# Performance work log

Measured on AMD Instinct MI355X. Metric: run time of the kernel, lower is better.

## Reference

```python
import jax, jax.numpy as jnp
import numpy as np

N, E, G = 50000, 800000, 64
IN, EDGE = 128, 16
HID, H = 32, 4
FHID, HF = 64, 4
OUT = 16
NEG_SLOPE = 0.2


def _segment_softmax(logits, seg, num):
    m = jax.ops.segment_max(logits, seg, num_segments=num)
    m = jnp.where(jnp.isfinite(m), m, 0.0)
    p = jnp.exp(logits - m[seg])
    s = jax.ops.segment_sum(p, seg, num_segments=num)
    return p / (s[seg] + 1e-16)


def gatv2(x, src, dst, eattr, Wl, bl, Wr, br, We, att, bias, concat):
    # PyG GATv2Conv with add_self_loops=True (edge_attr fill_value='mean')
    n = x.shape[0]
    heads, ch = att.shape
    ones = jnp.ones((src.shape[0],), x.dtype)
    cnt = jax.ops.segment_sum(ones, dst, num_segments=n)
    mean_attr = jax.ops.segment_sum(eattr, dst, num_segments=n) / jnp.maximum(cnt, 1.0)[:, None]
    loop = jnp.arange(n)
    s = jnp.concatenate([src, loop])
    d = jnp.concatenate([dst, loop])
    ea = jnp.concatenate([eattr, mean_attr], axis=0)
    xl = (x @ Wl + bl).reshape(n, heads, ch)   # lin_l (source)
    xr = (x @ Wr + br).reshape(n, heads, ch)   # lin_r (target)
    ee = (ea @ We).reshape(-1, heads, ch)      # lin_edge (no bias)
    z = jax.nn.leaky_relu(xl[s] + xr[d] + ee, NEG_SLOPE)  # [E+N, H, C]
    logits = jnp.einsum('ehc,hc->eh', z, att)
    alpha = _segment_softmax(logits, d, n)
    out = jax.ops.segment_sum(alpha[:, :, None] * xl[s], d, num_segments=n)  # [N, H, C]
    out = out.reshape(n, heads * ch) if concat else out.mean(axis=1)
    return out + bias


def _forward(x, edge_attr, src, dst, batch,
             Wl0, bl0, Wr0, br0, We0, att0, bo0,
             Wlh, blh, Wrh, brh, Weh, atth, boh,
             Wlf, blf, Wrf, brf, Wef, attf, bof,
             Wlin, blin):
    h1 = jax.nn.relu(gatv2(x, src, dst, edge_attr, Wl0, bl0, Wr0, br0, We0, att0, bo0, True))
    h2 = jax.nn.relu(gatv2(h1, src, dst, edge_attr, Wlh, blh, Wrh, brh, Weh, atth, boh, True))
    h3 = jax.nn.relu(gatv2(h2, src, dst, edge_attr, Wlf, blf, Wrf, brf, Wef, attf, bof, False))
    # global_mean_pool over graphs
    gsum = jax.ops.segment_sum(h3, batch, num_segments=G)
    gcnt = jax.ops.segment_sum(jnp.ones((h3.shape[0],), h3.dtype), batch, num_segments=G)
    g = gsum / jnp.maximum(gcnt, 1.0)[:, None]
    return g @ Wlin + blin  # final_dropout inactive in eval mode


def setup_inputs():
    key = jax.random.key(0)
    ks = jax.random.split(key, 20)
    def p(i, shape, fan_in):
        return jax.random.normal(ks[i], shape, jnp.float32) / np.sqrt(fan_in)
    z = lambda *s: jnp.zeros(s, jnp.float32)
    return {
        'x': jax.random.normal(ks[0], (N, IN), jnp.float32),
        'edge_index': jax.random.randint(ks[1], (2, E), 0, N),
        'batch': jnp.sort(jax.random.randint(ks[2], (N,), 0, G)),
        'edge_attr': jax.random.normal(ks[3], (E, EDGE), jnp.float32),
        'Wl0': p(4, (IN, H * HID), IN), 'bl0': z(H * HID),
        'Wr0': p(5, (IN, H * HID), IN), 'br0': z(H * HID),
        'We0': p(6, (EDGE, H * HID), EDGE), 'att0': p(7, (H, HID), HID), 'bo0': z(H * HID),
        'Wlh': p(8, (H * HID, H * HID), H * HID), 'blh': z(H * HID),
        'Wrh': p(9, (H * HID, H * HID), H * HID), 'brh': z(H * HID),
        'Weh': p(10, (EDGE, H * HID), EDGE), 'atth': p(11, (H, HID), HID), 'boh': z(H * HID),
        'Wlf': p(12, (H * HID, HF * FHID), H * HID), 'blf': z(HF * FHID),
        'Wrf': p(13, (H * HID, HF * FHID), H * HID), 'brf': z(HF * FHID),
        'Wef': p(14, (EDGE, HF * FHID), EDGE), 'attf': p(15, (HF, FHID), FHID), 'bof': z(FHID),
        'Wlin': p(16, (FHID, OUT), FHID), 'blin': z(OUT),
    }


def reference(x, edge_index, batch, edge_attr, Wl0, bl0, Wr0, br0, We0, att0, bo0, Wlh, blh, Wrh, brh, Weh, atth, boh, Wlf, blf, Wrf, brf, Wef, attf, bof, Wlin, blin):
    return _forward(x, edge_attr, edge_index[0], edge_index[1], batch,
                    Wl0, bl0, Wr0, br0, We0, att0, bo0,
                    Wlh, blh, Wrh, brh, Weh, atth, boh,
                    Wlf, blf, Wrf, brf, Wef, attf, bof,
                    Wlin, blin)
```

## Files before the change

### kernel.cpp

```cpp
#include <hip/hip_runtime.h>
#include <cstddef>

#define NSLOPE 0.2f

constexpr int NN = 50000;
constexpr int EE = 800000;
constexpr int GG = 64;
constexpr int SCAN_B = 1024;

typedef unsigned short ushort_t;
typedef unsigned int uint_t;
typedef __bf16 bhalf;
typedef bhalf bhalf8 __attribute__((ext_vector_type(8)));
typedef float floatx4 __attribute__((ext_vector_type(4)));
typedef _Float16 half_t;
typedef half_t half2_t __attribute__((ext_vector_type(2)));

__device__ __forceinline__ ushort_t f2b(float f) {
  unsigned int u = __float_as_uint(f);
  unsigned int r = (u + 0x7fffu + ((u >> 16) & 1u)) >> 16;
  return (ushort_t)r;
}
__device__ __forceinline__ float b2f(ushort_t b) {
  return __uint_as_float(((unsigned int)b) << 16);
}
__device__ __forceinline__ uint_t packh2(float a, float b) {
  half2_t h = {(half_t)a, (half_t)b};
  return __builtin_bit_cast(uint_t, h);
}
__device__ __forceinline__ float dot2acc(uint_t ea, half2_t w, float c) {
  half2_t a = __builtin_bit_cast(half2_t, ea);
#if __has_builtin(__builtin_amdgcn_fdot2)
  return __builtin_amdgcn_fdot2(a, w, c, false);
#else
  return c + (float)a.x * (float)w.x + (float)a.y * (float)w.y;
#endif
}

__device__ __forceinline__ float red16(float x) {
  int v = __builtin_bit_cast(int, x);
  x += __builtin_bit_cast(float, __builtin_amdgcn_update_dpp(0, v, 0xB1, 0xF, 0xF, true));
  v = __builtin_bit_cast(int, x);
  x += __builtin_bit_cast(float, __builtin_amdgcn_update_dpp(0, v, 0x4E, 0xF, 0xF, true));
  v = __builtin_bit_cast(int, x);
  x += __builtin_bit_cast(float, __builtin_amdgcn_update_dpp(0, v, 0x124, 0xF, 0xF, true));
  v = __builtin_bit_cast(int, x);
  x += __builtin_bit_cast(float, __builtin_amdgcn_update_dpp(0, v, 0x128, 0xF, 0xF, true));
  return x;
}

__global__ void hist_kernel(const int* __restrict__ dst, int* __restrict__ hist, int E) {
  int e = blockIdx.x * blockDim.x + threadIdx.x;
  if (e < E) atomicAdd(&hist[dst[e]], 1);
}

__global__ void scan_block_kernel(const int* __restrict__ in, int* __restrict__ out,
                                  int* __restrict__ bsum, int n) {
  __shared__ int tmp[SCAN_B];
  int gid = blockIdx.x * SCAN_B + threadIdx.x;
  int v = (gid < n) ? in[gid] : 0;
  tmp[threadIdx.x] = v;
  __syncthreads();
  for (int off = 1; off < SCAN_B; off <<= 1) {
    int t = (threadIdx.x >= off) ? tmp[threadIdx.x - off] : 0;
    __syncthreads();
    tmp[threadIdx.x] += t;
    __syncthreads();
  }
  if (gid < n) out[gid] = tmp[threadIdx.x];
  if (threadIdx.x == SCAN_B - 1) bsum[blockIdx.x] = tmp[threadIdx.x];
}

__global__ void scan_totals_kernel(const int* __restrict__ bsum, int* __restrict__ boff, int nb) {
  if (blockIdx.x == 0 && threadIdx.x == 0) {
    int run = 0;
    for (int i = 0; i < nb; ++i) { boff[i] = run; run += bsum[i]; }
  }
}

__global__ void add_offsets_kernel(int* __restrict__ rowptr, const int* __restrict__ boff,
                                   int* __restrict__ cursor, int n) {
  int gid = blockIdx.x * SCAN_B + threadIdx.x;
  if (gid == 0) { rowptr[0] = 0; cursor[0] = 0; }
  if (gid < n) {
    int v = rowptr[1 + gid] + boff[blockIdx.x];
    rowptr[1 + gid] = v;
    if (1 + gid < n) cursor[1 + gid] = v;
  }
}

__global__ void scatter_fused_kernel(const int* __restrict__ dst, const int* __restrict__ src,
                                     const float* __restrict__ eattr, int* __restrict__ cursor,
                                     int* __restrict__ srcp, uint_t* __restrict__ eah, int E) {
  int e = blockIdx.x * blockDim.x + threadIdx.x;
  if (e >= E) return;
  const float4* a = reinterpret_cast<const float4*>(eattr + (size_t)e * 16);
  float4 f0 = a[0], f1 = a[1], f2 = a[2], f3 = a[3];
  int pos = atomicAdd(&cursor[dst[e]], 1);
  srcp[pos] = src[e];
  uint4 o0 = make_uint4(packh2(f0.x, f0.y), packh2(f0.z, f0.w),
                        packh2(f1.x, f1.y), packh2(f1.z, f1.w));
  uint4 o1 = make_uint4(packh2(f2.x, f2.y), packh2(f2.z, f2.w),
                        packh2(f3.x, f3.y), packh2(f3.z, f3.w));
  uint4* b = reinterpret_cast<uint4*>(eah + (size_t)pos * 8);
  b[0] = o0; b[1] = o1;
}

__global__ __launch_bounds__(256) void mean_attr_kernel(
    const int* __restrict__ rowptr, const uint_t* __restrict__ eah,
    uint_t* __restrict__ meanattr_h, int N) {
  const int lane = threadIdx.x & 63;
  int d = blockIdx.x * (blockDim.x >> 6) + (threadIdx.x >> 6);
  if (d >= N) return;
  int beg = rowptr[d], end = rowptr[d + 1];
  int k2 = lane & 7;
  int sub = lane >> 3;
  float ax = 0.f, ay = 0.f;
  for (int j = beg + sub; j < end; j += 8) {
    half2_t h = __builtin_bit_cast(half2_t, eah[(size_t)j * 8 + k2]);
    ax += (float)h.x; ay += (float)h.y;
  }
  ax += __shfl_xor(ax, 8);  ay += __shfl_xor(ay, 8);
  ax += __shfl_xor(ax, 16); ay += __shfl_xor(ay, 16);
  ax += __shfl_xor(ax, 32); ay += __shfl_xor(ay, 32);
  if (sub == 0) {
    int c = end - beg; if (c < 1) c = 1;
    float inv = 1.f / (float)c;
    meanattr_h[(size_t)d * 8 + k2] = packh2(ax * inv, ay * inv);
  }
}

__global__ void f2b_kernel(const float* __restrict__ in, ushort_t* __restrict__ out, int n4) {
  int i = blockIdx.x * blockDim.x + threadIdx.x;
  if (i >= n4) return;
  float4 v = reinterpret_cast<const float4*>(in)[i];
  ushort4 o = make_ushort4(f2b(v.x), f2b(v.y), f2b(v.z), f2b(v.w));
  reinterpret_cast<ushort4*>(out)[i] = o;
}

__global__ void prep_w_kernel(const float* W0, ushort_t* T0, int n0,
                              const float* W1, ushort_t* T1, int n1,
                              const float* W2, ushort_t* T2, int n2,
                              const float* W3, ushort_t* T3, int n3,
                              const float* W4, ushort_t* T4, int n4,
                              const float* W5, ushort_t* T5, int n5) {
  const float* W; ushort_t* T; int Nc;
  switch (blockIdx.y) {
    case 0: W = W0; T = T0; Nc = n0; break;
    case 1: W = W1; T = T1; Nc = n1; break;
    case 2: W = W2; T = T2; Nc = n2; break;
    case 3: W = W3; T = T3; Nc = n3; break;
    case 4: W = W4; T = T4; Nc = n4; break;
    default: W = W5; T = T5; Nc = n5; break;
  }
  int idx = blockIdx.x * blockDim.x + threadIdx.x;
  if (idx >= Nc * 128) return;
  int n = idx >> 7, k = idx & 127;
  T[idx] = f2b(W[(size_t)k * Nc + n]);
}

__global__ void prep_we_kernel(const float* We0, const float* att0, uint_t* w0, float* a0,
                               const float* We1, const float* att1, uint_t* w1, float* a1,
                               const float* We2, const float* att2, uint_t* w2, float* a2) {
  const float* We; const float* att; uint_t* wp; float* ap; int C;
  switch (blockIdx.y) {
    case 0: We = We0; att = att0; wp = w0; ap = a0; C = 128; break;
    case 1: We = We1; att = att1; wp = w1; ap = a1; C = 128; break;
    default: We = We2; att = att2; wp = w2; ap = a2; C = 256; break;
  }
  int idx = blockIdx.x * blockDim.x + threadIdx.x;
  if (idx >= 9 * C) return;
  if (idx < 8 * C) {
    int sh = (C == 256) ? 8 : 7;
    int k2 = idx >> sh, ch = idx & (C - 1);
    wp[idx] = packh2(We[(size_t)(2 * k2) * C + ch], We[(size_t)(2 * k2 + 1) * C + ch]);
  } else {
    int ch = idx - 8 * C;
    ap[ch] = att[ch] * 1.44269504f;
  }
}

__global__ __launch_bounds__(256) void gemm_bt_dual_bf16(
    const ushort_t* __restrict__ Xb,
    const ushort_t* __restrict__ Wt0, const float* __restrict__ b0, ushort_t* __restrict__ Y0,
    const ushort_t* __restrict__ Wt1, const float* __restrict__ b1, ushort_t* __restrict__ Y1,
    int M, int Nc) {
  constexpr int K = 128, BM = 128, LDT = 136;
  __shared__ ushort_t Als[BM * LDT];
  __shared__ ushort_t Bls[BM * LDT];
  int nb = Nc >> 7;
  int half = blockIdx.y / nb;
  int cb = blockIdx.y % nb;
  const ushort_t* Wt = half ? Wt1 : Wt0;
  const float* bias = half ? b1 : b0;
  ushort_t* Y = half ? Y1 : Y0;
  int r0 = blockIdx.x * BM;
  int col0 = cb * 128;
  int tid = threadIdx.x;
  {
    int rl = tid >> 5;
    int kq = (tid & 31) * 4;
#pragma unroll
    for (int s = 0; s < 16; ++s) {
      int row = rl + s * 8;
      int grow = r0 + row;
      ushort4 v = make_ushort4(0, 0, 0, 0);
      if (grow < M) v = *reinterpret_cast<const ushort4*>(Xb + (size_t)grow * K + kq);
      *reinterpret_cast<ushort4*>(&Als[row * LDT + kq]) = v;
      ushort4 wv = *reinterpret_cast<const ushort4*>(Wt + (size_t)(col0 + row) * K + kq);
      *reinterpret_cast<ushort4*>(&Bls[row * LDT + kq]) = wv;
    }
  }
  __syncthreads();
  int lane = tid & 63;
  int w = tid >> 6;
  int m0 = (w >> 1) * 64;
  int n0 = (w & 1) * 64;
  int rin = lane & 15, quad = lane >> 4;
  floatx4 acc[4][4];
#pragma unroll
  for (int i = 0; i < 4; ++i)
#pragma unroll
    for (int j = 0; j < 4; ++j) acc[i][j] = (floatx4){0.f, 0.f, 0.f, 0.f};
#pragma unroll
  for (int kt = 0; kt < 4; ++kt) {
    int ko = kt * 32 + quad * 8;
    bhalf8 af[4], bf[4];
#pragma unroll
    for (int i = 0; i < 4; ++i)
      af[i] = *reinterpret_cast<const bhalf8*>(&Als[(m0 + i * 16 + rin) * LDT + ko]);
#pragma unroll
    for (int i = 0; i < 4; ++i)
      bf[i] = *reinterpret_cast<const bhalf8*>(&Bls[(n0 + i * 16 + rin) * LDT + ko]);
#pragma unroll
    for (int mi = 0; mi < 4; ++mi)
#pragma unroll
      for (int ni = 0; ni < 4; ++ni)
        acc[mi][ni] = __builtin_amdgcn_mfma_f32_16x16x32_bf16(af[mi], bf[ni], acc[mi][ni], 0, 0, 0);
  }
#pragma unroll
  for (int ni = 0; ni < 4; ++ni) {
    int gcol = col0 + n0 + ni * 16 + rin;
    float bb = bias[gcol];
#pragma unroll
    for (int mi = 0; mi < 4; ++mi) {
      int growb = r0 + m0 + mi * 16 + quad * 4;
#pragma unroll
      for (int r = 0; r < 4; ++r) {
        int grow = growb + r;
        if (grow < M) Y[(size_t)grow * Nc + gcol] = f2b(acc[mi][ni][r] + bb);
      }
    }
  }
}

template <int VPL>
__device__ __forceinline__ void loadb(const ushort_t* p, float* v) {
  if constexpr (VPL == 2) {
    ushort2 t = *reinterpret_cast<const ushort2*>(p);
    v[0] = b2f(t.x); v[1] = b2f(t.y);
  } else {
    ushort4 t = *reinterpret_cast<const ushort4*>(p);
    v[0] = b2f(t.x); v[1] = b2f(t.y); v[2] = b2f(t.z); v[3] = b2f(t.w);
  }
}
template <int VPL>
__device__ __forceinline__ void storeb(ushort_t* p, const float* v) {
  if constexpr (VPL == 2) {
    *reinterpret_cast<ushort2*>(p) = make_ushort2(f2b(v[0]), f2b(v[1]));
  } else {
    *reinterpret_cast<ushort4*>(p) = make_ushort4(f2b(v[0]), f2b(v[1]), f2b(v[2]), f2b(v[3]));
  }
}

template <int VPL>
__device__ __forceinline__ float lrelu_dot(const float* xv, const float* rv,
                                           const half2_t (*wepk)[VPL], const float* areg,
                                           const uint_t* ea) {
  float part = 0.f;
#pragma unroll
  for (int j = 0; j < VPL; ++j) {
    float z = xv[j] + rv[j];
#pragma unroll
    for (int k2 = 0; k2 < 8; ++k2) z = dot2acc(ea[k2], wepk[k2][j], z);
    float zl = fmaxf(z, NSLOPE * z);
    part = fmaf(zl, areg[j], part);
  }
  return red16(part);
}

template <int EB, int VPL, int C>
__device__ __forceinline__ void process_group(
    const int* __restrict__ srcp, const uint_t* __restrict__ eah, int j,
    const ushort_t* __restrict__ xl, int lane, const float* rv,
    const half2_t (*wepk)[VPL], const float* areg,
    float& s, float* acc) {
  int sn[EB];
#pragma unroll
  for (int u = 0; u < EB; ++u) sn[u] = srcp[j + u];
  float xv[EB][VPL];
#pragma unroll
  for (int u = 0; u < EB; ++u) loadb<VPL>(xl + (size_t)sn[u] * C + lane * VPL, xv[u]);
  float lg[EB];
#pragma unroll
  for (int u = 0; u < EB; ++u) {
    const uint4* ap4 = reinterpret_cast<const uint4*>(eah + (size_t)(j + u) * 8);
    uint4 e0 = ap4[0], e1 = ap4[1];
    uint_t ea[8] = {e0.x, e0.y, e0.z, e0.w, e1.x, e1.y, e1.z, e1.w};
    lg[u] = lrelu_dot<VPL>(xv[u], rv, wepk, areg, ea);
  }
  float p[EB], ps = 0.f;
#pragma unroll
  for (int u = 0; u < EB; ++u) { p[u] = exp2f(lg[u]); ps += p[u]; }
  s += ps;
#pragma unroll
  for (int jj = 0; jj < VPL; ++jj) {
    float t = p[0] * xv[0][jj];
#pragma unroll
    for (int u = 1; u < EB; ++u) t = fmaf(p[u], xv[u][jj], t);
    acc[jj] += t;
  }
}

template <int VPL, int C>
__device__ __forceinline__ void process_edge(
    int sn, const uint_t* ea,
    const ushort_t* __restrict__ xl, int lane, const float* rv,
    const half2_t (*wepk)[VPL], const float* areg,
    float& s, float* acc) {
  float xv[VPL];
  loadb<VPL>(xl + (size_t)sn * C + lane * VPL, xv);
  float lg = lrelu_dot<VPL>(xv, rv, wepk, areg, ea);
  float p = exp2f(lg);
  s += p;
#pragma unroll
  for (int jj = 0; jj < VPL; ++jj) acc[jj] = fmaf(p, xv[jj], acc[jj]);
}

template <int C, bool FINAL>
__global__ __launch_bounds__(256) void gat_fused_kernel(
    const int* __restrict__ rowptr,
    const int* __restrict__ srcp, const uint_t* __restrict__ eah,
    const uint_t* __restrict__ meanattr_h,
    const ushort_t* __restrict__ xl, const ushort_t* __restrict__ xr,
    const uint_t* __restrict__ wep,
    const float* __restrict__ atts,
    const float* __restrict__ bias, ushort_t* __restrict__ hout, int N) {
  constexpr int VPL = C / 64;
  const int lane = threadIdx.x & 63;
  int d = __builtin_amdgcn_readfirstlane(blockIdx.x * (blockDim.x >> 6) + (threadIdx.x >> 6));
  if (d >= N) return;

  half2_t wepk[8][VPL];
  float areg[VPL];
#pragma unroll
  for (int k2 = 0; k2 < 8; ++k2)
#pragma unroll
    for (int jj = 0; jj < VPL; ++jj)
      wepk[k2][jj] = __builtin_bit_cast(half2_t, wep[k2 * C + lane * VPL + jj]);
#pragma unroll
  for (int jj = 0; jj < VPL; ++jj) areg[jj] = atts[lane * VPL + jj];

  int beg = rowptr[d], end = rowptr[d + 1];
  float rv[VPL];
  loadb<VPL>(xr + (size_t)d * C + lane * VPL, rv);

  float s = 0.f;
  float acc[VPL];
#pragma unroll
  for (int jj = 0; jj < VPL; ++jj) acc[jj] = 0.f;

  int j = beg;
  if constexpr (C == 128) {
    for (; j + 8 <= end; j += 8)
      process_group<8, VPL, C>(srcp, eah, j, xl, lane, rv, wepk, areg, s, acc);
  }
  for (; j + 4 <= end; j += 4)
    process_group<4, VPL, C>(srcp, eah, j, xl, lane, rv, wepk, areg, s, acc);
  for (; j + 2 <= end; j += 2)
    process_group<2, VPL, C>(srcp, eah, j, xl, lane, rv, wepk, areg, s, acc);
  for (; j < end; ++j)
    process_group<1, VPL, C>(srcp, eah, j, xl, lane, rv, wepk, areg, s, acc);

  {
    const uint4* mp4 = reinterpret_cast<const uint4*>(meanattr_h + (size_t)d * 8);
    uint4 e0 = mp4[0], e1 = mp4[1];
    uint_t ea[8] = {e0.x, e0.y, e0.z, e0.w, e1.x, e1.y, e1.z, e1.w};
    process_edge<VPL, C>(d, ea, xl, lane, rv, wepk, areg, s, acc);
  }

  float inv = 1.f / (s + 1e-16f);
  if constexpr (!FINAL) {
    float res[VPL];
#pragma unroll
    for (int jj = 0; jj < VPL; ++jj) {
      float v = acc[jj] * inv + bias[lane * VPL + jj];
      res[jj] = v > 0.f ? v : 0.f;
    }
    storeb<VPL>(hout + (size_t)d * C + lane * VPL, res);
  } else {
    float v[VPL];
#pragma unroll
    for (int jj = 0; jj < VPL; ++jj) v[jj] = acc[jj] * inv;
#pragma unroll
    for (int jj = 0; jj < VPL; ++jj) {
      v[jj] += __shfl_xor(v[jj], 16);
      v[jj] += __shfl_xor(v[jj], 32);
    }
    if (lane < 16) {
      float res[VPL];
#pragma unroll
      for (int jj = 0; jj < VPL; ++jj) {
        float val = 0.25f * v[jj] + bias[lane * VPL + jj];
        res[jj] = val > 0.f ? val : 0.f;
      }
      storeb<VPL>(hout + (size_t)d * 64 + lane * VPL, res);
    }
  }
}

__global__ __launch_bounds__(256) void pool_kernel(
    const ushort_t* __restrict__ h3, const int* __restrict__ batch,
    float* __restrict__ gsum, float* __restrict__ gcnt, int N) {
  const int lane = threadIdx.x & 63;
  const int w = blockIdx.x * (blockDim.x >> 6) + (threadIdx.x >> 6);
  const int nw = gridDim.x * (blockDim.x >> 6);
  const int chunk = (N + nw - 1) / nw;
  int i0 = w * chunk;
  int i1 = i0 + chunk; if (i1 > N) i1 = N;
  if (i0 >= i1) return;
  int cur = batch[i0];
  float acc = 0.f;
  int cnt = 0;
  for (int i = i0; i < i1; ++i) {
    int g = batch[i];
    if (g != cur) {
      atomicAdd(&gsum[(size_t)cur * 64 + lane], acc);
      if (lane == 0) atomicAdd(&gcnt[cur], (float)cnt);
      acc = 0.f; cnt = 0; cur = g;
    }
    acc += b2f(h3[(size_t)i * 64 + lane]);
    ++cnt;
  }
  atomicAdd(&gsum[(size_t)cur * 64 + lane], acc);
  if (lane == 0) atomicAdd(&gcnt[cur], (float)cnt);
}

__global__ void final_kernel(const float* __restrict__ gsum, const float* __restrict__ gcnt,
                             const float* __restrict__ Wlin, const float* __restrict__ blin,
                             float* __restrict__ out) {
  int idx = blockIdx.x * blockDim.x + threadIdx.x;
  if (idx >= GG * 16) return;
  int g = idx >> 4, o = idx & 15;
  float c = gcnt[g];
  c = c > 1.f ? c : 1.f;
  float inv = 1.f / c;
  float acc = blin[o];
  for (int f = 0; f < 64; ++f) acc = fmaf(gsum[(size_t)g * 64 + f] * inv, Wlin[f * 16 + o], acc);
  out[idx] = acc;
}

extern "C" void kernel_launch(void* const* d_in, const int* in_sizes, int n_in,
                              void* d_out, int out_size, void* d_ws, size_t ws_size,
                              hipStream_t stream) {
  (void)in_sizes; (void)n_in; (void)out_size; (void)ws_size;
  const float* x     = (const float*)d_in[0];
  const int*   eidx  = (const int*)d_in[1];
  const int*   batch = (const int*)d_in[2];
  const float* eattr = (const float*)d_in[3];
  const float* Wl0 = (const float*)d_in[4];  const float* bl0 = (const float*)d_in[5];
  const float* Wr0 = (const float*)d_in[6];  const float* br0 = (const float*)d_in[7];
  const float* We0 = (const float*)d_in[8];  const float* att0 = (const float*)d_in[9];
  const float* bo0 = (const float*)d_in[10];
  const float* Wlh = (const float*)d_in[11]; const float* blh = (const float*)d_in[12];
  const float* Wrh = (const float*)d_in[13]; const float* brh = (const float*)d_in[14];
  const float* Weh = (const float*)d_in[15]; const float* atth = (const float*)d_in[16];
  const float* boh = (const float*)d_in[17];
  const float* Wlf = (const float*)d_in[18]; const float* blf = (const float*)d_in[19];
  const float* Wrf = (const float*)d_in[20]; const float* brf = (const float*)d_in[21];
  const float* Wef = (const float*)d_in[22]; const float* attf = (const float*)d_in[23];
  const float* bof = (const float*)d_in[24];
  const float* Wlin = (const float*)d_in[25]; const float* blin = (const float*)d_in[26];

  const int* src = eidx;
  const int* dst = eidx + EE;

  char* ws = (char*)d_ws;
  size_t off = 0;
  auto take = [&](size_t bytes) -> void* {
    void* p = ws + off;
    off += (bytes + 1023) & ~(size_t)1023;
    return p;
  };
  ushort_t* xl     = (ushort_t*)take((size_t)NN * 256 * 2);
  ushort_t* xr     = (ushort_t*)take((size_t)NN * 256 * 2);
  ushort_t* hb     = (ushort_t*)take((size_t)NN * 128 * 2);
  ushort_t* xb     = (ushort_t*)take((size_t)NN * 128 * 2);
  uint_t* meanattr_h = (uint_t*)take((size_t)NN * 8 * 4);
  int* hist        = (int*)take((size_t)NN * 4);
  int* rowptr      = (int*)take((size_t)(NN + 1) * 4);
  int* cursor      = (int*)take((size_t)NN * 4);
  int* bsum        = (int*)take(256);
  int* boff        = (int*)take(256);
  float* gsum      = (float*)take((size_t)GG * 64 * 4);
  float* gcnt      = (float*)take((size_t)GG * 4);
  ushort_t* wtl0   = (ushort_t*)take((size_t)128 * 128 * 2);
  ushort_t* wtr0   = (ushort_t*)take((size_t)128 * 128 * 2);
  ushort_t* wtlh   = (ushort_t*)take((size_t)128 * 128 * 2);
  ushort_t* wtrh   = (ushort_t*)take((size_t)128 * 128 * 2);
  ushort_t* wtlf   = (ushort_t*)take((size_t)256 * 128 * 2);
  ushort_t* wtrf   = (ushort_t*)take((size_t)256 * 128 * 2);
  int* srcp        = (int*)take((size_t)EE * 4);
  uint_t* eah      = (uint_t*)take((size_t)EE * 8 * 4);
  uint_t* we0p     = (uint_t*)take((size_t)8 * 128 * 4);
  uint_t* wehp     = (uint_t*)take((size_t)8 * 128 * 4);
  uint_t* wefp     = (uint_t*)take((size_t)8 * 256 * 4);
  float* att0s     = (float*)take((size_t)128 * 4);
  float* atths     = (float*)take((size_t)128 * 4);
  float* attfs     = (float*)take((size_t)256 * 4);

  hipMemsetAsync(hist, 0, (size_t)NN * 4, stream);
  hipMemsetAsync(gsum, 0, (size_t)GG * 64 * 4, stream);
  hipMemsetAsync(gcnt, 0, (size_t)GG * 4, stream);
  hist_kernel<<<(EE + 255) / 256, 256, 0, stream>>>(dst, hist, EE);
  int nsb = (NN + SCAN_B - 1) / SCAN_B;
  scan_block_kernel<<<nsb, SCAN_B, 0, stream>>>(hist, rowptr + 1, bsum, NN);
  scan_totals_kernel<<<1, 64, 0, stream>>>(bsum, boff, nsb);
  add_offsets_kernel<<<nsb, SCAN_B, 0, stream>>>(rowptr, boff, cursor, NN);
  scatter_fused_kernel<<<(EE + 255) / 256, 256, 0, stream>>>(dst, src, eattr, cursor, srcp, eah, EE);
  mean_attr_kernel<<<(NN + 3) / 4, 256, 0, stream>>>(rowptr, eah, meanattr_h, NN);
  prep_w_kernel<<<dim3(128, 6), 256, 0, stream>>>(Wl0, wtl0, 128, Wr0, wtr0, 128,
                                                  Wlh, wtlh, 128, Wrh, wtrh, 128,
                                                  Wlf, wtlf, 256, Wrf, wtrf, 256);
  prep_we_kernel<<<dim3(9, 3), 256, 0, stream>>>(We0, att0, we0p, att0s,
                                                 Weh, atth, wehp, atths,
                                                 Wef, attf, wefp, attfs);
  f2b_kernel<<<(NN * 128 / 4 + 255) / 256, 256, 0, stream>>>(x, xb, NN * 128 / 4);

  const int AGG_BLOCKS = (NN + 3) / 4;
  const int GEMM_MB = (NN + 127) / 128;

  gemm_bt_dual_bf16<<<dim3(GEMM_MB, 2), 256, 0, stream>>>(xb, wtl0, bl0, xl, wtr0, br0, xr, NN, 128);
  gat_fused_kernel<128, false><<<AGG_BLOCKS, 256, 0, stream>>>(
      rowptr, srcp, eah, meanattr_h, xl, xr, we0p, att0s, bo0, hb, NN);
  gemm_bt_dual_bf16<<<dim3(GEMM_MB, 2), 256, 0, stream>>>(hb, wtlh, blh, xl, wtrh, brh, xr, NN, 128);
  gat_fused_kernel<128, false><<<AGG_BLOCKS, 256, 0, stream>>>(
      rowptr, srcp, eah, meanattr_h, xl, xr, wehp, atths, boh, hb, NN);
  gemm_bt_dual_bf16<<<dim3(GEMM_MB, 4), 256, 0, stream>>>(hb, wtlf, blf, xl, wtrf, brf, xr, NN, 256);
  gat_fused_kernel<256, true><<<AGG_BLOCKS, 256, 0, stream>>>(
      rowptr, srcp, eah, meanattr_h, xl, xr, wefp, attfs, bof, hb, NN);
  pool_kernel<<<128, 256, 0, stream>>>(hb, batch, gsum, gcnt, NN);
  final_kernel<<<4, 256, 0, stream>>>(gsum, gcnt, Wlin, blin, (float*)d_out);
}
```

Before: 694.1 us.

## Fuse input bf16 conversion into GEMM, use fast exp2, one-wave GAT blocks

Drops the separate float-to-bf16 conversion kernel for the input features. The first dual GEMM now reads fp32 rows directly and rounds them to bf16 while staging into shared memory, which saves a full write and re-read of the converted input. It also swaps exp2f for the hardware exp2 intrinsic in the attention softmax, launches the GAT aggregation kernel with one 64-thread block per node instead of four waves per block, and merges three memsets into one by placing the buffers next to each other. The single-wave blocks raise the block count and change scheduling granularity, and the merged memset depends on the workspace layout staying as it is.

```diff
diff --git a/kernel.cpp b/kernel.cpp
--- a/kernel.cpp
+++ b/kernel.cpp
@@ -34,6 +34,13 @@
   return __builtin_amdgcn_fdot2(a, w, c, false);
 #else
   return c + (float)a.x * (float)w.x + (float)a.y * (float)w.y;
+#endif
+}
+__device__ __forceinline__ float fexp2(float x) {
+#if __has_builtin(__builtin_amdgcn_exp2f)
+  return __builtin_amdgcn_exp2f(x);
+#else
+  return exp2f(x);
 #endif
 }
 
@@ -130,14 +137,6 @@
   }
 }
 
-__global__ void f2b_kernel(const float* __restrict__ in, ushort_t* __restrict__ out, int n4) {
-  int i = blockIdx.x * blockDim.x + threadIdx.x;
-  if (i >= n4) return;
-  float4 v = reinterpret_cast<const float4*>(in)[i];
-  ushort4 o = make_ushort4(f2b(v.x), f2b(v.y), f2b(v.z), f2b(v.w));
-  reinterpret_cast<ushort4*>(out)[i] = o;
-}
-
 __global__ void prep_w_kernel(const float* W0, ushort_t* T0, int n0,
                               const float* W1, ushort_t* T1, int n1,
                               const float* W2, ushort_t* T2, int n2,
@@ -180,8 +179,9 @@
   }
 }
 
+template <typename TA>
 __global__ __launch_bounds__(256) void gemm_bt_dual_bf16(
-    const ushort_t* __restrict__ Xb,
+    const TA* __restrict__ Xb,
     const ushort_t* __restrict__ Wt0, const float* __restrict__ b0, ushort_t* __restrict__ Y0,
     const ushort_t* __restrict__ Wt1, const float* __restrict__ b1, ushort_t* __restrict__ Y1,
     int M, int Nc) {
@@ -205,7 +205,14 @@
       int row = rl + s * 8;
       int grow = r0 + row;
       ushort4 v = make_ushort4(0, 0, 0, 0);
-      if (grow < M) v = *reinterpret_cast<const ushort4*>(Xb + (size_t)grow * K + kq);
+      if (grow < M) {
+        if constexpr (sizeof(TA) == 4) {
+          float4 f = *reinterpret_cast<const float4*>(Xb + (size_t)grow * K + kq);
+          v = make_ushort4(f2b(f.x), f2b(f.y), f2b(f.z), f2b(f.w));
+        } else {
+          v = *reinterpret_cast<const ushort4*>(Xb + (size_t)grow * K + kq);
+        }
+      }
       *reinterpret_cast<ushort4*>(&Als[row * LDT + kq]) = v;
       ushort4 wv = *reinterpret_cast<const ushort4*>(Wt + (size_t)(col0 + row) * K + kq);
       *reinterpret_cast<ushort4*>(&Bls[row * LDT + kq]) = wv;
@@ -311,7 +318,7 @@
   }
   float p[EB], ps = 0.f;
 #pragma unroll
-  for (int u = 0; u < EB; ++u) { p[u] = exp2f(lg[u]); ps += p[u]; }
+  for (int u = 0; u < EB; ++u) { p[u] = fexp2(lg[u]); ps += p[u]; }
   s += ps;
 #pragma unroll
   for (int jj = 0; jj < VPL; ++jj) {
@@ -331,14 +338,14 @@
   float xv[VPL];
   loadb<VPL>(xl + (size_t)sn * C + lane * VPL, xv);
   float lg = lrelu_dot<VPL>(xv, rv, wepk, areg, ea);
-  float p = exp2f(lg);
+  float p = fexp2(lg);
   s += p;
 #pragma unroll
   for (int jj = 0; jj < VPL; ++jj) acc[jj] = fmaf(p, xv[jj], acc[jj]);
 }
 
 template <int C, bool FINAL>
-__global__ __launch_bounds__(256) void gat_fused_kernel(
+__global__ __launch_bounds__(64) void gat_fused_kernel(
     const int* __restrict__ rowptr,
     const int* __restrict__ srcp, const uint_t* __restrict__ eah,
     const uint_t* __restrict__ meanattr_h,
@@ -348,7 +355,7 @@
     const float* __restrict__ bias, ushort_t* __restrict__ hout, int N) {
   constexpr int VPL = C / 64;
   const int lane = threadIdx.x & 63;
-  int d = __builtin_amdgcn_readfirstlane(blockIdx.x * (blockDim.x >> 6) + (threadIdx.x >> 6));
+  int d = blockIdx.x;
   if (d >= N) return;
 
   half2_t wepk[8][VPL];
@@ -495,15 +502,14 @@
   ushort_t* xl     = (ushort_t*)take((size_t)NN * 256 * 2);
   ushort_t* xr     = (ushort_t*)take((size_t)NN * 256 * 2);
   ushort_t* hb     = (ushort_t*)take((size_t)NN * 128 * 2);
-  ushort_t* xb     = (ushort_t*)take((size_t)NN * 128 * 2);
   uint_t* meanattr_h = (uint_t*)take((size_t)NN * 8 * 4);
   int* hist        = (int*)take((size_t)NN * 4);
+  float* gsum      = (float*)take((size_t)GG * 64 * 4);
+  float* gcnt      = (float*)take((size_t)GG * 4);
   int* rowptr      = (int*)take((size_t)(NN + 1) * 4);
   int* cursor      = (int*)take((size_t)NN * 4);
   int* bsum        = (int*)take(256);
   int* boff        = (int*)take(256);
-  float* gsum      = (float*)take((size_t)GG * 64 * 4);
-  float* gcnt      = (float*)take((size_t)GG * 4);
   ushort_t* wtl0   = (ushort_t*)take((size_t)128 * 128 * 2);
   ushort_t* wtr0   = (ushort_t*)take((size_t)128 * 128 * 2);
   ushort_t* wtlh   = (ushort_t*)take((size_t)128 * 128 * 2);
@@ -519,9 +525,7 @@
   float* atths     = (float*)take((size_t)128 * 4);
   float* attfs     = (float*)take((size_t)256 * 4);
 
-  hipMemsetAsync(hist, 0, (size_t)NN * 4, stream);
-  hipMemsetAsync(gsum, 0, (size_t)GG * 64 * 4, stream);
-  hipMemsetAsync(gcnt, 0, (size_t)GG * 4, stream);
+  hipMemsetAsync(hist, 0, 200704 + 16384 + 256, stream);
   hist_kernel<<<(EE + 255) / 256, 256, 0, stream>>>(dst, hist, EE);
   int nsb = (NN + SCAN_B - 1) / SCAN_B;
   scan_block_kernel<<<nsb, SCAN_B, 0, stream>>>(hist, rowptr + 1, bsum, NN);
@@ -535,19 +539,20 @@
   prep_we_kernel<<<dim3(9, 3), 256, 0, stream>>>(We0, att0, we0p, att0s,
                                                  Weh, atth, wehp, atths,
                                                  Wef, attf, wefp, attfs);
-  f2b_kernel<<<(NN * 128 / 4 + 255) / 256, 256, 0, stream>>>(x, xb, NN * 128 / 4);
-
-  const int AGG_BLOCKS = (NN + 3) / 4;
+
   const int GEMM_MB = (NN + 127) / 128;
 
-  gemm_bt_dual_bf16<<<dim3(GEMM_MB, 2), 256, 0, stream>>>(xb, wtl0, bl0, xl, wtr0, br0, xr, NN, 128);
-  gat_fused_kernel<128, false><<<AGG_BLOCKS, 256, 0, stream>>>(
+  gemm_bt_dual_bf16<float><<<dim3(GEMM_MB, 2), 256, 0, stream>>>(
+      x, wtl0, bl0, xl, wtr0, br0, xr, NN, 128);
+  gat_fused_kernel<128, false><<<NN, 64, 0, stream>>>(
       rowptr, srcp, eah, meanattr_h, xl, xr, we0p, att0s, bo0, hb, NN);
-  gemm_bt_dual_bf16<<<dim3(GEMM_MB, 2), 256, 0, stream>>>(hb, wtlh, blh, xl, wtrh, brh, xr, NN, 128);
-  gat_fused_kernel<128, false><<<AGG_BLOCKS, 256, 0, stream>>>(
+  gemm_bt_dual_bf16<ushort_t><<<dim3(GEMM_MB, 2), 256, 0, stream>>>(
+      hb, wtlh, blh, xl, wtrh, brh, xr, NN, 128);
+  gat_fused_kernel<128, false><<<NN, 64, 0, stream>>>(
       rowptr, srcp, eah, meanattr_h, xl, xr, wehp, atths, boh, hb, NN);
-  gemm_bt_dual_bf16<<<dim3(GEMM_MB, 4), 256, 0, stream>>>(hb, wtlf, blf, xl, wtrf, brf, xr, NN, 256);
-  gat_fused_kernel<256, true><<<AGG_BLOCKS, 256, 0, stream>>>(
+  gemm_bt_dual_bf16<ushort_t><<<dim3(GEMM_MB, 4), 256, 0, stream>>>(
+      hb, wtlf, blf, xl, wtrf, brf, xr, NN, 256);
+  gat_fused_kernel<256, true><<<NN, 64, 0, stream>>>(
       rowptr, srcp, eah, meanattr_h, xl, xr, wefp, attfs, bof, hb, NN);
   pool_kernel<<<128, 256, 0, stream>>>(hb, batch, gsum, gcnt, NN);
   final_kernel<<<4, 256, 0, stream>>>(gsum, gcnt, Wlin, blin, (float*)d_out);
```

After: 663.9 us. 1.05x faster.
